# Optimization experiments

Measured on AMD Instinct MI355X. Metric: run time of the kernel, lower is better.

Reference implementation:

```python
import jax, jax.numpy as jnp
import numpy as np

N_NODES = 50000
N_EDGES = 1_600_000
IN_F = 128
OUT_F = 32
HEADS = 4
EDGE_F = 4
EDGE_HID = 32


def setup_inputs() -> dict:
    key = jax.random.key(0)
    ks = jax.random.split(key, 12)
    x = jax.random.normal(ks[0], (N_NODES, IN_F), dtype=jnp.float32)
    edge_index = jax.random.randint(ks[1], (2, N_EDGES), 0, N_NODES, dtype=jnp.int32)
    edge_attr = jax.random.normal(ks[2], (N_EDGES, EDGE_F), dtype=jnp.float32)
    # linear: in_features -> heads*out_features (stored as [in, out] for x @ W)
    W = jax.random.normal(ks[3], (IN_F, HEADS * OUT_F), dtype=jnp.float32) * (1.0 / np.sqrt(IN_F))
    b = jnp.zeros((HEADS * OUT_F,), dtype=jnp.float32)
    # edge_proj: Linear(EDGE_F,32) -> ReLU -> Linear(32, heads)
    eW1 = jax.random.normal(ks[4], (EDGE_F, EDGE_HID), dtype=jnp.float32) * (1.0 / np.sqrt(EDGE_F))
    eb1 = jnp.zeros((EDGE_HID,), dtype=jnp.float32)
    eW2 = jax.random.normal(ks[5], (EDGE_HID, HEADS), dtype=jnp.float32) * (1.0 / np.sqrt(EDGE_HID))
    eb2 = jnp.zeros((HEADS,), dtype=jnp.float32)
    att_src = jax.random.normal(ks[6], (1, HEADS, OUT_F), dtype=jnp.float32) * 0.1
    att_dst = jax.random.normal(ks[7], (1, HEADS, OUT_F), dtype=jnp.float32) * 0.1
    return {"x": x, "edge_index": edge_index, "edge_attr": edge_attr,
            "W": W, "b": b, "eW1": eW1, "eb1": eb1, "eW2": eW2, "eb2": eb2,
            "att_src": att_src, "att_dst": att_dst}


def reference(x, edge_index, edge_attr, W, b, eW1, eb1, eW2, eb2, att_src, att_dst):
    N = x.shape[0]
    src, dst = edge_index[0], edge_index[1]
    E = src.shape[0]

    h = (x @ W + b).reshape(N, HEADS, OUT_F)                     # [N,H,F]
    alpha_src = jnp.sum(h[src] * att_src, axis=-1)               # [E,H]
    alpha_dst = jnp.sum(h[dst] * att_dst, axis=-1)               # [E,H]
    edge_att = jax.nn.relu(edge_attr @ eW1 + eb1) @ eW2 + eb2    # [E,H]
    alpha = jax.nn.leaky_relu(alpha_src + alpha_dst + edge_att, negative_slope=0.2)

    # softmax_by_src: dense [N,H] buffer of -inf, scatter-set by src
    # softmax over the NODE axis, then gather back per edge.
    last = jax.ops.segment_max(jnp.arange(E, dtype=jnp.int32), src, num_segments=N)  # [N]
    valid = last >= 0
    dense = jnp.where(valid[:, None], alpha[jnp.clip(last, 0)], -jnp.inf)  # [N,H]
    dense = jax.nn.softmax(dense, axis=0)
    alpha_e = dense[src]                                         # [E,H]

    # dropout: module default training=False path (identity), eval mode
    # scatter-add aggregation: out[src] += h[dst] * alpha_e (all heads at once)
    msg = h[dst] * alpha_e[:, :, None]                           # [E,H,F]
    out = jnp.zeros_like(h).at[src].add(msg)                     # [N,H,F]
    return out.mean(axis=1)                                      # [N,F]
```

## Files before the change

### kernel.cpp

```cpp
#include <hip/hip_runtime.h>
#include <hip/hip_fp16.h>
#include <math.h>


#define SUPCAP 9216
#define AGG_CAP 2048
#define BIN_CHUNK 2048

__global__ __launch_bounds__(256, 3) void k_pre(
    const float* __restrict__ x, const float* __restrict__ W,
    const float* __restrict__ b, const float* __restrict__ att_src,
    const float* __restrict__ att_dst, __half* __restrict__ hbuf16,
    float* __restrict__ s_, float* __restrict__ t_,
    const int* __restrict__ src, const int* __restrict__ dst,
    int* __restrict__ bcur, unsigned* __restrict__ bin_y,
    unsigned* __restrict__ bin_e,
    int N, int E, int nsup, int ngemm, int nbin) {
  __shared__ __align__(16) float smem[12672];
  int tx = threadIdx.x;
  int bid = blockIdx.x;
  int mmin = (nbin < ngemm) ? nbin : ngemm;
  int m2 = 2 * mmin;
  bool isbin;
  int wid;
  if (bid < m2) { isbin = (bid & 1); wid = bid >> 1; }
  else { isbin = (nbin > ngemm); wid = mmin + (bid - m2); }

  if (isbin) {
    uint2* ebuf = (uint2*)smem;
    int* hist = (int*)(smem + 4096);
    int* bas  = hist + 256;
    int* curs = bas + 256;
    int* gpos = curs + 256;
    int e0 = wid * BIN_CHUNK;
    int n = E - e0; if (n > BIN_CHUNK) n = BIN_CHUNK;
    hist[tx] = 0;
    __syncthreads();
    for (int i = tx; i < n; i += 256) {
      atomicAdd(&hist[src[e0 + i] >> 8], 1);
    }
    __syncthreads();
    int v = hist[tx];
    bas[tx] = v;
    __syncthreads();
    for (int off = 1; off < 256; off <<= 1) {
      int t = (tx >= off) ? bas[tx - off] : 0;
      __syncthreads();
      bas[tx] += t;
      __syncthreads();
    }
    curs[tx] = bas[tx] - v;
    if (tx < nsup && v > 0) gpos[tx] = atomicAdd(&bcur[tx], v);
    __syncthreads();
    for (int i = tx; i < n; i += 256) {
      int e = e0 + i;
      int s = src[e], d = dst[e];
      int pos = atomicAdd(&curs[s >> 8], 1);
      unsigned loc = (unsigned)(s & 255);
      ebuf[pos] = make_uint2((loc << 24) | (unsigned)e, (loc << 16) | (unsigned)d);
    }
    __syncthreads();
    for (int i = tx; i < n; i += 256) {
      uint2 w = ebuf[i];
      int lo = 0, hi = 255;
      while (lo < hi) {
        int mid = (lo + hi) >> 1;
        if (bas[mid] > i) hi = mid; else lo = mid + 1;
      }
      int bb = lo;
      int lbase = bas[bb] - hist[bb];
      int off = gpos[bb] + (i - lbase);
      if (off < SUPCAP) {
        bin_e[(size_t)bb * SUPCAP + off] = w.x;
        bin_y[(size_t)bb * SUPCAP + off] = w.y;
      }
    }
  } else {
    float* xs = smem;
    float* ws = smem + 64 * 132;
    int r0 = wid * 64;
    const float4* xg = (const float4*)(x + (size_t)r0 * 128);
#pragma unroll
    for (int j = 0; j < 8; ++j) {
      int l = tx + j * 256;
      int row = l >> 5, col4 = l & 31;
      float4 v = make_float4(0.f, 0.f, 0.f, 0.f);
      if (r0 + row < N) v = xg[l];
      *(float4*)(xs + row * 132 + col4 * 4) = v;
    }
    int cg = tx & 15, rg = tx >> 4;
    float acc[4][8];
#pragma unroll
    for (int r = 0; r < 4; ++r)
#pragma unroll
      for (int c = 0; c < 8; ++c) acc[r][c] = 0.f;
    const float4* Wg4 = (const float4*)W;
    const float* xbase = xs + rg * 4 * 132;
    int woff = cg * 8 + ((cg >> 3) << 2);
    for (int kt = 0; kt < 4; ++kt) {
      __syncthreads();
#pragma unroll
      for (int j = 0; j < 4; ++j) {
        int ll = tx + j * 256;
        int row = ll >> 5, c4 = ll & 31;
        *(float4*)(ws + row * 132 + c4 * 4 + ((c4 >> 4) << 2)) = Wg4[kt * 1024 + ll];
      }
      __syncthreads();
#pragma unroll 2
      for (int k4 = 0; k4 < 8; ++k4) {
        float4 xr0 = *(const float4*)(xbase + kt * 32 + k4 * 4);
        float4 xr1 = *(const float4*)(xbase + 132 + kt * 32 + k4 * 4);
        float4 xr2 = *(const float4*)(xbase + 264 + kt * 32 + k4 * 4);
        float4 xr3 = *(const float4*)(xbase + 396 + kt * 32 + k4 * 4);
#pragma unroll
        for (int kk = 0; kk < 4; ++kk) {
          const float* wrow = ws + (k4 * 4 + kk) * 132 + woff;
          float4 w0 = *(const float4*)(wrow);
          float4 w1 = *(const float4*)(wrow + 4);
          const float wc[8] = {w0.x, w0.y, w0.z, w0.w, w1.x, w1.y, w1.z, w1.w};
          float xv0 = ((const float*)&xr0)[kk];
          float xv1 = ((const float*)&xr1)[kk];
          float xv2 = ((const float*)&xr2)[kk];
          float xv3 = ((const float*)&xr3)[kk];
#pragma unroll
          for (int c = 0; c < 8; ++c) {
            acc[0][c] += xv0 * wc[c];
            acc[1][c] += xv1 * wc[c];
            acc[2][c] += xv2 * wc[c];
            acc[3][c] += xv3 * wc[c];
          }
        }
      }
    }
    float4 b0 = ((const float4*)b)[cg * 2],       b1 = ((const float4*)b)[cg * 2 + 1];
    float4 s0 = ((const float4*)att_src)[cg * 2], s1 = ((const float4*)att_src)[cg * 2 + 1];
    float4 d0 = ((const float4*)att_dst)[cg * 2], d1 = ((const float4*)att_dst)[cg * 2 + 1];
    const float bbv[8] = {b0.x, b0.y, b0.z, b0.w, b1.x, b1.y, b1.z, b1.w};
    const float asv[8] = {s0.x, s0.y, s0.z, s0.w, s1.x, s1.y, s1.z, s1.w};
    const float adv[8] = {d0.x, d0.y, d0.z, d0.w, d1.x, d1.y, d1.z, d1.w};
    int hd = cg >> 2;
#pragma unroll
    for (int r = 0; r < 4; ++r) {
      float o[8];
#pragma unroll
      for (int c = 0; c < 8; ++c) o[c] = acc[r][c] + bbv[c];
      float sp = 0.f, tp = 0.f;
#pragma unroll
      for (int c = 0; c < 8; ++c) { sp += o[c] * asv[c]; tp += o[c] * adv[c]; }
      sp += __shfl_xor(sp, 1); sp += __shfl_xor(sp, 2);
      tp += __shfl_xor(tp, 1); tp += __shfl_xor(tp, 2);
      int grow = r0 + rg * 4 + r;
      if (grow < N) {
        __half2 h0 = __floats2half2_rn(o[0], o[1]);
        __half2 h1 = __floats2half2_rn(o[2], o[3]);
        __half2 h2 = __floats2half2_rn(o[4], o[5]);
        __half2 h3 = __floats2half2_rn(o[6], o[7]);
        uint4 u;
        u.x = *(unsigned*)&h0; u.y = *(unsigned*)&h1;
        u.z = *(unsigned*)&h2; u.w = *(unsigned*)&h3;
        ((uint4*)(hbuf16 + (size_t)grow * 128))[cg] = u;
        if ((tx & 3) == 0) {
          s_[grow * 4 + hd] = sp;
          t_[grow * 4 + hd] = tp;
        }
      }
    }
  }
}

__global__ __launch_bounds__(256) void k_dense(
    const int* __restrict__ bcur, const unsigned* __restrict__ bin_e,
    const unsigned* __restrict__ bin_y,
    const int* __restrict__ dst, const float* __restrict__ edge_attr,
    const float* __restrict__ eW1, const float* __restrict__ eb1,
    const float* __restrict__ eW2, const float* __restrict__ eb2,
    const float* __restrict__ s_, const float* __restrict__ t_,
    float* __restrict__ dense, float* __restrict__ pmax,
    float* __restrict__ psum,
    unsigned short* __restrict__ sorted_dst,
    int* __restrict__ noff, int* __restrict__ ncnt, int N) {
  __shared__ int lastv[256];
  __shared__ int hist[256], bas[256], curs[256];
  __shared__ float lm[256 * 4], ls[256 * 4];
  int sp = blockIdx.x, tx = threadIdx.x;
  lastv[tx] = -1;
  hist[tx] = 0;
  __syncthreads();
  int cnt = bcur[sp]; if (cnt > SUPCAP) cnt = SUPCAP;
  const unsigned* be = bin_e + (size_t)sp * SUPCAP;
  const unsigned* by = bin_y + (size_t)sp * SUPCAP;
  for (int i = tx; i < cnt; i += 256) {
    unsigned p = be[i];
    atomicMax(&lastv[p >> 24], (int)(p & 0xFFFFFF));
    atomicAdd(&hist[by[i] >> 16], 1);
  }
  __syncthreads();
  int v = hist[tx];
  bas[tx] = v;
  __syncthreads();
  for (int off = 1; off < 256; off <<= 1) {
    int t = (tx >= off) ? bas[tx - off] : 0;
    __syncthreads();
    bas[tx] += t;
    __syncthreads();
  }
  curs[tx] = bas[tx] - v;
  int gn = sp * 256 + tx;
  noff[gn] = sp * SUPCAP + bas[tx] - v;
  ncnt[gn] = v;
  __syncthreads();
  unsigned short* sd = sorted_dst + (size_t)sp * SUPCAP;
  for (int i = tx; i < cnt; i += 256) {
    unsigned y = by[i];
    int pos = atomicAdd(&curs[y >> 16], 1);
    sd[pos] = (unsigned short)y;
  }
  float vv[4] = {-INFINITY, -INFINITY, -INFINITY, -INFINITY};
  if (gn < N) {
    int e = lastv[tx];
    if (e >= 0) {
      int d = dst[e];
      const float* ea = edge_attr + (size_t)e * 4;
      float e0 = ea[0], e1 = ea[1], e2 = ea[2], e3 = ea[3];
      float a0 = eb2[0], a1 = eb2[1], a2 = eb2[2], a3 = eb2[3];
#pragma unroll
      for (int i = 0; i < 32; ++i) {
        float hid = eb1[i] + e0 * eW1[i] + e1 * eW1[32 + i] + e2 * eW1[64 + i] + e3 * eW1[96 + i];
        hid = fmaxf(hid, 0.f);
        a0 += hid * eW2[i * 4 + 0]; a1 += hid * eW2[i * 4 + 1];
        a2 += hid * eW2[i * 4 + 2]; a3 += hid * eW2[i * 4 + 3];
      }
      float w0 = s_[gn * 4 + 0] + t_[d * 4 + 0] + a0;
      float w1 = s_[gn * 4 + 1] + t_[d * 4 + 1] + a1;
      float w2 = s_[gn * 4 + 2] + t_[d * 4 + 2] + a2;
      float w3 = s_[gn * 4 + 3] + t_[d * 4 + 3] + a3;
      vv[0] = w0 > 0.f ? w0 : 0.2f * w0;
      vv[1] = w1 > 0.f ? w1 : 0.2f * w1;
      vv[2] = w2 > 0.f ? w2 : 0.2f * w2;
      vv[3] = w3 > 0.f ? w3 : 0.2f * w3;
    }
#pragma unroll
    for (int h = 0; h < 4; ++h) dense[gn * 4 + h] = vv[h];
  }
#pragma unroll
  for (int h = 0; h < 4; ++h) {
    lm[tx * 4 + h] = vv[h];
    ls[tx * 4 + h] = (vv[h] > -INFINITY) ? 1.f : 0.f;
  }
  __syncthreads();
  for (int off = 128; off > 0; off >>= 1) {
    if (tx < off) {
#pragma unroll
      for (int h = 0; h < 4; ++h) {
        float m2 = lm[(tx + off) * 4 + h], s2 = ls[(tx + off) * 4 + h];
        float m1 = lm[tx * 4 + h], s1 = ls[tx * 4 + h];
        float M = fmaxf(m1, m2);
        if (M > -INFINITY) {
          ls[tx * 4 + h] = s1 * expf(m1 - M) + s2 * expf(m2 - M);
          lm[tx * 4 + h] = M;
        }
      }
    }
    __syncthreads();
  }
  if (tx == 0) {
#pragma unroll
    for (int h = 0; h < 4; ++h) {
      pmax[sp * 4 + h] = lm[h];
      psum[sp * 4 + h] = ls[h];
    }
  }
}

#define ACC(r, P, Q) { \
  float2 f0 = __half22float2(*(__half2*)&r.x), f1 = __half22float2(*(__half2*)&r.y); \
  float2 f2 = __half22float2(*(__half2*)&r.z), f3 = __half22float2(*(__half2*)&r.w); \
  P.x += f0.x; P.y += f0.y; P.z += f1.x; P.w += f1.y; \
  Q.x += f2.x; Q.y += f2.y; Q.z += f3.x; Q.w += f3.y; }

__global__ __launch_bounds__(256) void k_agg(
    const unsigned short* __restrict__ sorted_dst,
    const int* __restrict__ noff, const int* __restrict__ ncnt,
    const __half* __restrict__ hbuf16, const float* __restrict__ dense,
    const float* __restrict__ pmax, const float* __restrict__ psum, int nb,
    float* __restrict__ out, int N) {
  __shared__ unsigned short sl[AGG_CAP];
  __shared__ float lm[256], ls[256];
  __shared__ float sgm[4], sgi[4];
  int tx = threadIdx.x;
  int n0 = blockIdx.x << 4;
  int nlast = n0 + 15; if (nlast > N - 1) nlast = N - 1;
  int lstart = noff[n0];
  int lend = noff[nlast] + ncnt[nlast];
  int total = lend - lstart; if (total > AGG_CAP) total = AGG_CAP;
  for (int i = tx; i < total; i += 256) sl[i] = sorted_dst[lstart + i];
  {
    int h = tx & 3, chunk = tx >> 2;
    float m = -INFINITY, s = 0.f;
    for (int bq = chunk; bq < nb; bq += 64) {
      float m2 = pmax[bq * 4 + h], s2 = psum[bq * 4 + h];
      float M = fmaxf(m, m2);
      if (M > -INFINITY) {
        s = s * expf(m - M) + s2 * expf(m2 - M);
        m = M;
      }
    }
    lm[tx] = m; ls[tx] = s;
    __syncthreads();
    for (int off = 128; off >= 4; off >>= 1) {
      if (tx < off) {
        float m2 = lm[tx + off], s2 = ls[tx + off];
        float m1 = lm[tx], s1 = ls[tx];
        float M = fmaxf(m1, m2);
        if (M > -INFINITY) {
          ls[tx] = s1 * expf(m1 - M) + s2 * expf(m2 - M);
          lm[tx] = M;
        }
      }
      __syncthreads();
    }
    if (tx < 4) {
      sgm[tx] = lm[tx];
      sgi[tx] = 1.f / ls[tx];
    }
    __syncthreads();
  }
  int g = tx >> 4, l = tx & 15;
  int n = n0 + g;
  if (n >= N) return;
  int beg = noff[n] - lstart;
  int cnt = ncnt[n];
  if (beg + cnt > total) cnt = total - beg;
  int end = beg + cnt;
  int hd = l >> 2;
  float w = expf(dense[(size_t)n * 4 + hd] - sgm[hd]) * sgi[hd];
  float4 p0 = {0, 0, 0, 0}, q0 = {0, 0, 0, 0};
  float4 p1 = {0, 0, 0, 0}, q1 = {0, 0, 0, 0};
  int e = beg;
  for (; e + 7 < end; e += 8) {
    int c0 = sl[e],     c1 = sl[e + 1], c2 = sl[e + 2], c3 = sl[e + 3];
    int c4_ = sl[e + 4], c5 = sl[e + 5], c6 = sl[e + 6], c7 = sl[e + 7];
    uint4 r0 = *((const uint4*)(hbuf16 + ((size_t)c0  << 7)) + l);
    uint4 r1 = *((const uint4*)(hbuf16 + ((size_t)c1  << 7)) + l);
    uint4 r2 = *((const uint4*)(hbuf16 + ((size_t)c2  << 7)) + l);
    uint4 r3 = *((const uint4*)(hbuf16 + ((size_t)c3  << 7)) + l);
    uint4 r4 = *((const uint4*)(hbuf16 + ((size_t)c4_ << 7)) + l);
    uint4 r5 = *((const uint4*)(hbuf16 + ((size_t)c5  << 7)) + l);
    uint4 r6 = *((const uint4*)(hbuf16 + ((size_t)c6  << 7)) + l);
    uint4 r7 = *((const uint4*)(hbuf16 + ((size_t)c7  << 7)) + l);
    ACC(r0, p0, q0); ACC(r1, p1, q1); ACC(r2, p0, q0); ACC(r3, p1, q1);
    ACC(r4, p0, q0); ACC(r5, p1, q1); ACC(r6, p0, q0); ACC(r7, p1, q1);
  }
  for (; e + 3 < end; e += 4) {
    int c0 = sl[e], c1 = sl[e + 1], c2 = sl[e + 2], c3 = sl[e + 3];
    uint4 r0 = *((const uint4*)(hbuf16 + ((size_t)c0 << 7)) + l);
    uint4 r1 = *((const uint4*)(hbuf16 + ((size_t)c1 << 7)) + l);
    uint4 r2 = *((const uint4*)(hbuf16 + ((size_t)c2 << 7)) + l);
    uint4 r3 = *((const uint4*)(hbuf16 + ((size_t)c3 << 7)) + l);
    ACC(r0, p0, q0); ACC(r1, p1, q1); ACC(r2, p0, q0); ACC(r3, p1, q1);
  }
  for (; e < end; ++e) {
    int c0 = sl[e];
    uint4 r0 = *((const uint4*)(hbuf16 + ((size_t)c0 << 7)) + l);
    ACC(r0, p0, q0);
  }
  p0.x += p1.x; p0.y += p1.y; p0.z += p1.z; p0.w += p1.w;
  q0.x += q1.x; q0.y += q1.y; q0.z += q1.z; q0.w += q1.w;
  p0.x *= w; p0.y *= w; p0.z *= w; p0.w *= w;
  q0.x *= w; q0.y *= w; q0.z *= w; q0.w *= w;
  p0.x += __shfl_xor(p0.x, 4);  p0.y += __shfl_xor(p0.y, 4);
  p0.z += __shfl_xor(p0.z, 4);  p0.w += __shfl_xor(p0.w, 4);
  q0.x += __shfl_xor(q0.x, 4);  q0.y += __shfl_xor(q0.y, 4);
  q0.z += __shfl_xor(q0.z, 4);  q0.w += __shfl_xor(q0.w, 4);
  p0.x += __shfl_xor(p0.x, 8);  p0.y += __shfl_xor(p0.y, 8);
  p0.z += __shfl_xor(p0.z, 8);  p0.w += __shfl_xor(p0.w, 8);
  q0.x += __shfl_xor(q0.x, 8);  q0.y += __shfl_xor(q0.y, 8);
  q0.z += __shfl_xor(q0.z, 8);  q0.w += __shfl_xor(q0.w, 8);
  if (l < 4) {
    float4 oA, oB;
    oA.x = 0.25f * p0.x; oA.y = 0.25f * p0.y; oA.z = 0.25f * p0.z; oA.w = 0.25f * p0.w;
    oB.x = 0.25f * q0.x; oB.y = 0.25f * q0.y; oB.z = 0.25f * q0.z; oB.w = 0.25f * q0.w;
    *(float4*)(out + (size_t)n * 32 + l * 8) = oA;
    *(float4*)(out + (size_t)n * 32 + l * 8 + 4) = oB;
  }
}

extern "C" void kernel_launch(void* const* d_in, const int* in_sizes, int n_in,
                              void* d_out, int out_size, void* d_ws, size_t ws_size,
                              hipStream_t stream) {
  const float* x        = (const float*)d_in[0];
  const int*   ei       = (const int*)d_in[1];
  const float* edge_attr= (const float*)d_in[2];
  const float* W        = (const float*)d_in[3];
  const float* b        = (const float*)d_in[4];
  const float* eW1      = (const float*)d_in[5];
  const float* eb1      = (const float*)d_in[6];
  const float* eW2      = (const float*)d_in[7];
  const float* eb2      = (const float*)d_in[8];
  const float* att_src  = (const float*)d_in[9];
  const float* att_dst  = (const float*)d_in[10];
  float* out = (float*)d_out;

  const int N = in_sizes[0] / 128;
  const int E = in_sizes[1] / 2;
  const int* src = ei;
  const int* dst = ei + E;
  const int NSUP = (N + 255) >> 8;

  char* wp = (char*)d_ws;
  auto alloc = [&](size_t bytes) -> void* {
    void* p = (void*)wp;
    wp += (bytes + 255) & ~(size_t)255;
    return p;
  };
  __half* hbuf16 = (__half*)alloc((size_t)N * 128 * 2);
  float* s_    = (float*)alloc((size_t)N * 4 * 4);
  float* t_    = (float*)alloc((size_t)N * 4 * 4);
  float* dense = (float*)alloc((size_t)N * 4 * 4);
  float* pmax  = (float*)alloc((size_t)NSUP * 4 * 4);
  float* psum  = (float*)alloc((size_t)NSUP * 4 * 4);
  int* bcur    = (int*)alloc((size_t)NSUP * 4);
  unsigned* bin_y = (unsigned*)alloc((size_t)NSUP * SUPCAP * 4);
  unsigned* bin_e = (unsigned*)alloc((size_t)NSUP * SUPCAP * 4);
  unsigned short* sorted_dst = (unsigned short*)alloc((size_t)NSUP * SUPCAP * 2);
  int* noff    = (int*)alloc((size_t)NSUP * 256 * 4);
  int* ncnt    = (int*)alloc((size_t)NSUP * 256 * 4);

  const int NGEMM = (N + 63) / 64;
  const int NBIN  = (E + BIN_CHUNK - 1) / BIN_CHUNK;

  hipMemsetAsync(bcur, 0, (size_t)NSUP * 4, stream);
  k_pre<<<NGEMM + NBIN, 256, 0, stream>>>(x, W, b, att_src, att_dst, hbuf16, s_, t_,
                                          src, dst, bcur, bin_y, bin_e,
                                          N, E, NSUP, NGEMM, NBIN);
  k_dense<<<NSUP, 256, 0, stream>>>(bcur, bin_e, bin_y, dst, edge_attr, eW1, eb1, eW2, eb2,
                                    s_, t_, dense, pmax, psum, sorted_dst, noff, ncnt, N);
  k_agg<<<(N + 15) / 16, 256, 0, stream>>>(sorted_dst, noff, ncnt, hbuf16, dense,
                                           pmax, psum, NSUP, out, N);
}
```

Baseline: 239.3 us.

## Fuse three kernels into one persistent kernel with software grid barriers

Merges the GEMM/binning, dense softmax, and aggregation kernels into a single persistent kernel sized to occupancy times CU count. Work items are grid-strided and phases are separated by an atomic-counter grid barrier, removing two kernel launch gaps and their tail effects. The GEMM tile shrinks from 64 to 32 rows to fit reduced shared memory and allow 4 blocks per CU. The risk is barrier spin overhead and load imbalance, plus deadlock if not all blocks are co-resident.

```diff
diff --git a/kernel.cpp b/kernel.cpp
--- a/kernel.cpp
+++ b/kernel.cpp
@@ -7,381 +7,404 @@
 #define AGG_CAP 2048
 #define BIN_CHUNK 2048
 
-__global__ __launch_bounds__(256, 3) void k_pre(
+__device__ __forceinline__ void gsync(int* bar, int nblk) {
+  __syncthreads();
+  if (threadIdx.x == 0) {
+    __threadfence();
+    int g = __hip_atomic_load(&bar[1], __ATOMIC_RELAXED, __HIP_MEMORY_SCOPE_AGENT);
+    int a = __hip_atomic_fetch_add(&bar[0], 1, __ATOMIC_ACQ_REL, __HIP_MEMORY_SCOPE_AGENT);
+    if (a == nblk - 1) {
+      __hip_atomic_store(&bar[0], 0, __ATOMIC_RELAXED, __HIP_MEMORY_SCOPE_AGENT);
+      __hip_atomic_fetch_add(&bar[1], 1, __ATOMIC_RELEASE, __HIP_MEMORY_SCOPE_AGENT);
+    } else {
+      while (__hip_atomic_load(&bar[1], __ATOMIC_ACQUIRE, __HIP_MEMORY_SCOPE_AGENT) == g)
+        __builtin_amdgcn_s_sleep(8);
+    }
+    __threadfence();
+  }
+  __syncthreads();
+}
+
+#define ACC(r, P, Q) { \
+  float2 f0 = __half22float2(*(__half2*)&r.x), f1 = __half22float2(*(__half2*)&r.y); \
+  float2 f2 = __half22float2(*(__half2*)&r.z), f3 = __half22float2(*(__half2*)&r.w); \
+  P.x += f0.x; P.y += f0.y; P.z += f1.x; P.w += f1.y; \
+  Q.x += f2.x; Q.y += f2.y; Q.z += f3.x; Q.w += f3.y; }
+
+__global__ __launch_bounds__(256, 4) void k_fused(
     const float* __restrict__ x, const float* __restrict__ W,
     const float* __restrict__ b, const float* __restrict__ att_src,
     const float* __restrict__ att_dst, __half* __restrict__ hbuf16,
     float* __restrict__ s_, float* __restrict__ t_,
     const int* __restrict__ src, const int* __restrict__ dst,
+    const float* __restrict__ edge_attr,
+    const float* __restrict__ eW1, const float* __restrict__ eb1,
+    const float* __restrict__ eW2, const float* __restrict__ eb2,
     int* __restrict__ bcur, unsigned* __restrict__ bin_y,
     unsigned* __restrict__ bin_e,
-    int N, int E, int nsup, int ngemm, int nbin) {
-  __shared__ __align__(16) float smem[12672];
-  int tx = threadIdx.x;
-  int bid = blockIdx.x;
-  int mmin = (nbin < ngemm) ? nbin : ngemm;
-  int m2 = 2 * mmin;
-  bool isbin;
-  int wid;
-  if (bid < m2) { isbin = (bid & 1); wid = bid >> 1; }
-  else { isbin = (nbin > ngemm); wid = mmin + (bid - m2); }
-
-  if (isbin) {
-    uint2* ebuf = (uint2*)smem;
-    int* hist = (int*)(smem + 4096);
-    int* bas  = hist + 256;
-    int* curs = bas + 256;
-    int* gpos = curs + 256;
-    int e0 = wid * BIN_CHUNK;
-    int n = E - e0; if (n > BIN_CHUNK) n = BIN_CHUNK;
-    hist[tx] = 0;
-    __syncthreads();
-    for (int i = tx; i < n; i += 256) {
-      atomicAdd(&hist[src[e0 + i] >> 8], 1);
-    }
-    __syncthreads();
-    int v = hist[tx];
-    bas[tx] = v;
-    __syncthreads();
-    for (int off = 1; off < 256; off <<= 1) {
-      int t = (tx >= off) ? bas[tx - off] : 0;
-      __syncthreads();
-      bas[tx] += t;
-      __syncthreads();
-    }
-    curs[tx] = bas[tx] - v;
-    if (tx < nsup && v > 0) gpos[tx] = atomicAdd(&bcur[tx], v);
-    __syncthreads();
-    for (int i = tx; i < n; i += 256) {
-      int e = e0 + i;
-      int s = src[e], d = dst[e];
-      int pos = atomicAdd(&curs[s >> 8], 1);
-      unsigned loc = (unsigned)(s & 255);
-      ebuf[pos] = make_uint2((loc << 24) | (unsigned)e, (loc << 16) | (unsigned)d);
-    }
-    __syncthreads();
-    for (int i = tx; i < n; i += 256) {
-      uint2 w = ebuf[i];
-      int lo = 0, hi = 255;
-      while (lo < hi) {
-        int mid = (lo + hi) >> 1;
-        if (bas[mid] > i) hi = mid; else lo = mid + 1;
-      }
-      int bb = lo;
-      int lbase = bas[bb] - hist[bb];
-      int off = gpos[bb] + (i - lbase);
-      if (off < SUPCAP) {
-        bin_e[(size_t)bb * SUPCAP + off] = w.x;
-        bin_y[(size_t)bb * SUPCAP + off] = w.y;
-      }
-    }
-  } else {
-    float* xs = smem;
-    float* ws = smem + 64 * 132;
-    int r0 = wid * 64;
-    const float4* xg = (const float4*)(x + (size_t)r0 * 128);
-#pragma unroll
-    for (int j = 0; j < 8; ++j) {
-      int l = tx + j * 256;
-      int row = l >> 5, col4 = l & 31;
-      float4 v = make_float4(0.f, 0.f, 0.f, 0.f);
-      if (r0 + row < N) v = xg[l];
-      *(float4*)(xs + row * 132 + col4 * 4) = v;
-    }
-    int cg = tx & 15, rg = tx >> 4;
-    float acc[4][8];
-#pragma unroll
-    for (int r = 0; r < 4; ++r)
-#pragma unroll
-      for (int c = 0; c < 8; ++c) acc[r][c] = 0.f;
-    const float4* Wg4 = (const float4*)W;
-    const float* xbase = xs + rg * 4 * 132;
-    int woff = cg * 8 + ((cg >> 3) << 2);
-    for (int kt = 0; kt < 4; ++kt) {
-      __syncthreads();
-#pragma unroll
-      for (int j = 0; j < 4; ++j) {
-        int ll = tx + j * 256;
-        int row = ll >> 5, c4 = ll & 31;
-        *(float4*)(ws + row * 132 + c4 * 4 + ((c4 >> 4) << 2)) = Wg4[kt * 1024 + ll];
-      }
-      __syncthreads();
-#pragma unroll 2
-      for (int k4 = 0; k4 < 8; ++k4) {
-        float4 xr0 = *(const float4*)(xbase + kt * 32 + k4 * 4);
-        float4 xr1 = *(const float4*)(xbase + 132 + kt * 32 + k4 * 4);
-        float4 xr2 = *(const float4*)(xbase + 264 + kt * 32 + k4 * 4);
-        float4 xr3 = *(const float4*)(xbase + 396 + kt * 32 + k4 * 4);
-#pragma unroll
-        for (int kk = 0; kk < 4; ++kk) {
-          const float* wrow = ws + (k4 * 4 + kk) * 132 + woff;
-          float4 w0 = *(const float4*)(wrow);
-          float4 w1 = *(const float4*)(wrow + 4);
-          const float wc[8] = {w0.x, w0.y, w0.z, w0.w, w1.x, w1.y, w1.z, w1.w};
-          float xv0 = ((const float*)&xr0)[kk];
-          float xv1 = ((const float*)&xr1)[kk];
-          float xv2 = ((const float*)&xr2)[kk];
-          float xv3 = ((const float*)&xr3)[kk];
-#pragma unroll
-          for (int c = 0; c < 8; ++c) {
-            acc[0][c] += xv0 * wc[c];
-            acc[1][c] += xv1 * wc[c];
-            acc[2][c] += xv2 * wc[c];
-            acc[3][c] += xv3 * wc[c];
-          }
-        }
-      }
-    }
-    float4 b0 = ((const float4*)b)[cg * 2],       b1 = ((const float4*)b)[cg * 2 + 1];
-    float4 s0 = ((const float4*)att_src)[cg * 2], s1 = ((const float4*)att_src)[cg * 2 + 1];
-    float4 d0 = ((const float4*)att_dst)[cg * 2], d1 = ((const float4*)att_dst)[cg * 2 + 1];
-    const float bbv[8] = {b0.x, b0.y, b0.z, b0.w, b1.x, b1.y, b1.z, b1.w};
-    const float asv[8] = {s0.x, s0.y, s0.z, s0.w, s1.x, s1.y, s1.z, s1.w};
-    const float adv[8] = {d0.x, d0.y, d0.z, d0.w, d1.x, d1.y, d1.z, d1.w};
-    int hd = cg >> 2;
-#pragma unroll
-    for (int r = 0; r < 4; ++r) {
-      float o[8];
-#pragma unroll
-      for (int c = 0; c < 8; ++c) o[c] = acc[r][c] + bbv[c];
-      float sp = 0.f, tp = 0.f;
-#pragma unroll
-      for (int c = 0; c < 8; ++c) { sp += o[c] * asv[c]; tp += o[c] * adv[c]; }
-      sp += __shfl_xor(sp, 1); sp += __shfl_xor(sp, 2);
-      tp += __shfl_xor(tp, 1); tp += __shfl_xor(tp, 2);
-      int grow = r0 + rg * 4 + r;
-      if (grow < N) {
-        __half2 h0 = __floats2half2_rn(o[0], o[1]);
-        __half2 h1 = __floats2half2_rn(o[2], o[3]);
-        __half2 h2 = __floats2half2_rn(o[4], o[5]);
-        __half2 h3 = __floats2half2_rn(o[6], o[7]);
-        uint4 u;
-        u.x = *(unsigned*)&h0; u.y = *(unsigned*)&h1;
-        u.z = *(unsigned*)&h2; u.w = *(unsigned*)&h3;
-        ((uint4*)(hbuf16 + (size_t)grow * 128))[cg] = u;
-        if ((tx & 3) == 0) {
-          s_[grow * 4 + hd] = sp;
-          t_[grow * 4 + hd] = tp;
-        }
-      }
-    }
-  }
-}
-
-__global__ __launch_bounds__(256) void k_dense(
-    const int* __restrict__ bcur, const unsigned* __restrict__ bin_e,
-    const unsigned* __restrict__ bin_y,
-    const int* __restrict__ dst, const float* __restrict__ edge_attr,
-    const float* __restrict__ eW1, const float* __restrict__ eb1,
-    const float* __restrict__ eW2, const float* __restrict__ eb2,
-    const float* __restrict__ s_, const float* __restrict__ t_,
+    unsigned short* __restrict__ sorted_dst,
+    int* __restrict__ noff, int* __restrict__ ncnt,
     float* __restrict__ dense, float* __restrict__ pmax,
-    float* __restrict__ psum,
-    unsigned short* __restrict__ sorted_dst,
-    int* __restrict__ noff, int* __restrict__ ncnt, int N) {
-  __shared__ int lastv[256];
-  __shared__ int hist[256], bas[256], curs[256];
-  __shared__ float lm[256 * 4], ls[256 * 4];
-  int sp = blockIdx.x, tx = threadIdx.x;
-  lastv[tx] = -1;
-  hist[tx] = 0;
-  __syncthreads();
-  int cnt = bcur[sp]; if (cnt > SUPCAP) cnt = SUPCAP;
-  const unsigned* be = bin_e + (size_t)sp * SUPCAP;
-  const unsigned* by = bin_y + (size_t)sp * SUPCAP;
-  for (int i = tx; i < cnt; i += 256) {
-    unsigned p = be[i];
-    atomicMax(&lastv[p >> 24], (int)(p & 0xFFFFFF));
-    atomicAdd(&hist[by[i] >> 16], 1);
-  }
-  __syncthreads();
-  int v = hist[tx];
-  bas[tx] = v;
-  __syncthreads();
-  for (int off = 1; off < 256; off <<= 1) {
-    int t = (tx >= off) ? bas[tx - off] : 0;
-    __syncthreads();
-    bas[tx] += t;
-    __syncthreads();
-  }
-  curs[tx] = bas[tx] - v;
-  int gn = sp * 256 + tx;
-  noff[gn] = sp * SUPCAP + bas[tx] - v;
-  ncnt[gn] = v;
-  __syncthreads();
-  unsigned short* sd = sorted_dst + (size_t)sp * SUPCAP;
-  for (int i = tx; i < cnt; i += 256) {
-    unsigned y = by[i];
-    int pos = atomicAdd(&curs[y >> 16], 1);
-    sd[pos] = (unsigned short)y;
-  }
-  float vv[4] = {-INFINITY, -INFINITY, -INFINITY, -INFINITY};
-  if (gn < N) {
-    int e = lastv[tx];
-    if (e >= 0) {
-      int d = dst[e];
-      const float* ea = edge_attr + (size_t)e * 4;
-      float e0 = ea[0], e1 = ea[1], e2 = ea[2], e3 = ea[3];
-      float a0 = eb2[0], a1 = eb2[1], a2 = eb2[2], a3 = eb2[3];
-#pragma unroll
-      for (int i = 0; i < 32; ++i) {
-        float hid = eb1[i] + e0 * eW1[i] + e1 * eW1[32 + i] + e2 * eW1[64 + i] + e3 * eW1[96 + i];
-        hid = fmaxf(hid, 0.f);
-        a0 += hid * eW2[i * 4 + 0]; a1 += hid * eW2[i * 4 + 1];
-        a2 += hid * eW2[i * 4 + 2]; a3 += hid * eW2[i * 4 + 3];
-      }
-      float w0 = s_[gn * 4 + 0] + t_[d * 4 + 0] + a0;
-      float w1 = s_[gn * 4 + 1] + t_[d * 4 + 1] + a1;
-      float w2 = s_[gn * 4 + 2] + t_[d * 4 + 2] + a2;
-      float w3 = s_[gn * 4 + 3] + t_[d * 4 + 3] + a3;
-      vv[0] = w0 > 0.f ? w0 : 0.2f * w0;
-      vv[1] = w1 > 0.f ? w1 : 0.2f * w1;
-      vv[2] = w2 > 0.f ? w2 : 0.2f * w2;
-      vv[3] = w3 > 0.f ? w3 : 0.2f * w3;
-    }
-#pragma unroll
-    for (int h = 0; h < 4; ++h) dense[gn * 4 + h] = vv[h];
-  }
-#pragma unroll
-  for (int h = 0; h < 4; ++h) {
-    lm[tx * 4 + h] = vv[h];
-    ls[tx * 4 + h] = (vv[h] > -INFINITY) ? 1.f : 0.f;
-  }
-  __syncthreads();
-  for (int off = 128; off > 0; off >>= 1) {
-    if (tx < off) {
-#pragma unroll
-      for (int h = 0; h < 4; ++h) {
-        float m2 = lm[(tx + off) * 4 + h], s2 = ls[(tx + off) * 4 + h];
-        float m1 = lm[tx * 4 + h], s1 = ls[tx * 4 + h];
-        float M = fmaxf(m1, m2);
-        if (M > -INFINITY) {
-          ls[tx * 4 + h] = s1 * expf(m1 - M) + s2 * expf(m2 - M);
-          lm[tx * 4 + h] = M;
-        }
-      }
-    }
-    __syncthreads();
-  }
-  if (tx == 0) {
-#pragma unroll
-    for (int h = 0; h < 4; ++h) {
-      pmax[sp * 4 + h] = lm[h];
-      psum[sp * 4 + h] = ls[h];
-    }
-  }
-}
-
-#define ACC(r, P, Q) { \
-  float2 f0 = __half22float2(*(__half2*)&r.x), f1 = __half22float2(*(__half2*)&r.y); \
-  float2 f2 = __half22float2(*(__half2*)&r.z), f3 = __half22float2(*(__half2*)&r.w); \
-  P.x += f0.x; P.y += f0.y; P.z += f1.x; P.w += f1.y; \
-  Q.x += f2.x; Q.y += f2.y; Q.z += f3.x; Q.w += f3.y; }
-
-__global__ __launch_bounds__(256) void k_agg(
-    const unsigned short* __restrict__ sorted_dst,
-    const int* __restrict__ noff, const int* __restrict__ ncnt,
-    const __half* __restrict__ hbuf16, const float* __restrict__ dense,
-    const float* __restrict__ pmax, const float* __restrict__ psum, int nb,
-    float* __restrict__ out, int N) {
-  __shared__ unsigned short sl[AGG_CAP];
-  __shared__ float lm[256], ls[256];
+    float* __restrict__ psum, float* __restrict__ out,
+    int N, int E, int nsup, int ngemm, int nbin, int nagg,
+    int phases, int* bar) {
+  __shared__ __align__(16) float smem[8448];
   __shared__ float sgm[4], sgi[4];
   int tx = threadIdx.x;
-  int n0 = blockIdx.x << 4;
-  int nlast = n0 + 15; if (nlast > N - 1) nlast = N - 1;
-  int lstart = noff[n0];
-  int lend = noff[nlast] + ncnt[nlast];
-  int total = lend - lstart; if (total > AGG_CAP) total = AGG_CAP;
-  for (int i = tx; i < total; i += 256) sl[i] = sorted_dst[lstart + i];
-  {
-    int h = tx & 3, chunk = tx >> 2;
-    float m = -INFINITY, s = 0.f;
-    for (int bq = chunk; bq < nb; bq += 64) {
-      float m2 = pmax[bq * 4 + h], s2 = psum[bq * 4 + h];
-      float M = fmaxf(m, m2);
-      if (M > -INFINITY) {
-        s = s * expf(m - M) + s2 * expf(m2 - M);
-        m = M;
+  int bid = blockIdx.x, G = gridDim.x;
+  bool fused = (phases == 7);
+
+  if (phases & 1) {
+    int nitems = ngemm + nbin;
+    int mmin = (nbin < ngemm) ? nbin : ngemm;
+    int m2 = 2 * mmin;
+    for (int j = bid; j < nitems; j += G) {
+      __syncthreads();
+      bool isbin; int wid;
+      if (j < m2) { isbin = (j & 1); wid = j >> 1; }
+      else { isbin = (nbin > ngemm); wid = mmin + (j - m2); }
+      if (isbin) {
+        uint2* ebuf = (uint2*)smem;
+        int* hist = (int*)(smem + 4096);
+        int* bas  = hist + 256;
+        int* curs = bas + 256;
+        int* gpos = curs + 256;
+        int e0 = wid * BIN_CHUNK;
+        int n = E - e0; if (n > BIN_CHUNK) n = BIN_CHUNK;
+        hist[tx] = 0;
+        __syncthreads();
+        for (int i = tx; i < n; i += 256) {
+          atomicAdd(&hist[src[e0 + i] >> 8], 1);
+        }
+        __syncthreads();
+        int v = hist[tx];
+        bas[tx] = v;
+        __syncthreads();
+        for (int off = 1; off < 256; off <<= 1) {
+          int t = (tx >= off) ? bas[tx - off] : 0;
+          __syncthreads();
+          bas[tx] += t;
+          __syncthreads();
+        }
+        curs[tx] = bas[tx] - v;
+        if (tx < nsup && v > 0) gpos[tx] = atomicAdd(&bcur[tx], v);
+        __syncthreads();
+        for (int i = tx; i < n; i += 256) {
+          int e = e0 + i;
+          int s = src[e], d = dst[e];
+          int pos = atomicAdd(&curs[s >> 8], 1);
+          unsigned loc = (unsigned)(s & 255);
+          ebuf[pos] = make_uint2((loc << 24) | (unsigned)e, (loc << 16) | (unsigned)d);
+        }
+        __syncthreads();
+        for (int i = tx; i < n; i += 256) {
+          uint2 w = ebuf[i];
+          int lo = 0, hi = 255;
+          while (lo < hi) {
+            int mid = (lo + hi) >> 1;
+            if (bas[mid] > i) hi = mid; else lo = mid + 1;
+          }
+          int bb = lo;
+          int lbase = bas[bb] - hist[bb];
+          int off = gpos[bb] + (i - lbase);
+          if (off < SUPCAP) {
+            bin_e[(size_t)bb * SUPCAP + off] = w.x;
+            bin_y[(size_t)bb * SUPCAP + off] = w.y;
+          }
+        }
+      } else {
+        float* xs = smem;
+        float* ws = smem + 4224;
+        int r0 = wid * 32;
+        const float4* xg = (const float4*)(x + (size_t)r0 * 128);
+#pragma unroll
+        for (int j2 = 0; j2 < 4; ++j2) {
+          int l = tx + j2 * 256;
+          int row = l >> 5, col4 = l & 31;
+          float4 v = make_float4(0.f, 0.f, 0.f, 0.f);
+          if (r0 + row < N) v = xg[l];
+          *(float4*)(xs + row * 132 + col4 * 4) = v;
+        }
+        int cg = tx & 15, rg = tx >> 4;
+        float acc[2][8];
+#pragma unroll
+        for (int r = 0; r < 2; ++r)
+#pragma unroll
+          for (int c = 0; c < 8; ++c) acc[r][c] = 0.f;
+        const float4* Wg4 = (const float4*)W;
+        const float* xbase = xs + rg * 2 * 132;
+        int woff = cg * 8 + ((cg >> 3) << 2);
+        for (int kt = 0; kt < 4; ++kt) {
+          __syncthreads();
+#pragma unroll
+          for (int j2 = 0; j2 < 4; ++j2) {
+            int ll = tx + j2 * 256;
+            int row = ll >> 5, c4 = ll & 31;
+            *(float4*)(ws + row * 132 + c4 * 4 + ((c4 >> 4) << 2)) = Wg4[kt * 1024 + ll];
+          }
+          __syncthreads();
+#pragma unroll 2
+          for (int k4 = 0; k4 < 8; ++k4) {
+            float4 xr0 = *(const float4*)(xbase + kt * 32 + k4 * 4);
+            float4 xr1 = *(const float4*)(xbase + 132 + kt * 32 + k4 * 4);
+#pragma unroll
+            for (int kk = 0; kk < 4; ++kk) {
+              const float* wrow = ws + (k4 * 4 + kk) * 132 + woff;
+              float4 w0 = *(const float4*)(wrow);
+              float4 w1 = *(const float4*)(wrow + 4);
+              const float wc[8] = {w0.x, w0.y, w0.z, w0.w, w1.x, w1.y, w1.z, w1.w};
+              float xv0 = ((const float*)&xr0)[kk];
+              float xv1 = ((const float*)&xr1)[kk];
+#pragma unroll
+              for (int c = 0; c < 8; ++c) {
+                acc[0][c] += xv0 * wc[c];
+                acc[1][c] += xv1 * wc[c];
+              }
+            }
+          }
+        }
+        float4 b0 = ((const float4*)b)[cg * 2],       b1 = ((const float4*)b)[cg * 2 + 1];
+        float4 s0 = ((const float4*)att_src)[cg * 2], s1 = ((const float4*)att_src)[cg * 2 + 1];
+        float4 d0 = ((const float4*)att_dst)[cg * 2], d1 = ((const float4*)att_dst)[cg * 2 + 1];
+        const float bbv[8] = {b0.x, b0.y, b0.z, b0.w, b1.x, b1.y, b1.z, b1.w};
+        const float asv[8] = {s0.x, s0.y, s0.z, s0.w, s1.x, s1.y, s1.z, s1.w};
+        const float adv[8] = {d0.x, d0.y, d0.z, d0.w, d1.x, d1.y, d1.z, d1.w};
+        int hd = cg >> 2;
+#pragma unroll
+        for (int r = 0; r < 2; ++r) {
+          float o[8];
+#pragma unroll
+          for (int c = 0; c < 8; ++c) o[c] = acc[r][c] + bbv[c];
+          float sp = 0.f, tp = 0.f;
+#pragma unroll
+          for (int c = 0; c < 8; ++c) { sp += o[c] * asv[c]; tp += o[c] * adv[c]; }
+          sp += __shfl_xor(sp, 1); sp += __shfl_xor(sp, 2);
+          tp += __shfl_xor(tp, 1); tp += __shfl_xor(tp, 2);
+          int grow = r0 + rg * 2 + r;
+          if (grow < N) {
+            __half2 h0 = __floats2half2_rn(o[0], o[1]);
+            __half2 h1 = __floats2half2_rn(o[2], o[3]);
+            __half2 h2 = __floats2half2_rn(o[4], o[5]);
+            __half2 h3 = __floats2half2_rn(o[6], o[7]);
+            uint4 u;
+            u.x = *(unsigned*)&h0; u.y = *(unsigned*)&h1;
+            u.z = *(unsigned*)&h2; u.w = *(unsigned*)&h3;
+            ((uint4*)(hbuf16 + (size_t)grow * 128))[cg] = u;
+            if ((tx & 3) == 0) {
+              s_[grow * 4 + hd] = sp;
+              t_[grow * 4 + hd] = tp;
+            }
+          }
+        }
       }
     }
-    lm[tx] = m; ls[tx] = s;
-    __syncthreads();
-    for (int off = 128; off >= 4; off >>= 1) {
-      if (tx < off) {
-        float m2 = lm[tx + off], s2 = ls[tx + off];
-        float m1 = lm[tx], s1 = ls[tx];
-        float M = fmaxf(m1, m2);
+  }
+  if (fused) gsync(bar, G);
+
+  if (phases & 2) {
+    int* lastv = (int*)smem;
+    int* hist  = (int*)(smem + 256);
+    int* bas   = (int*)(smem + 512);
+    int* curs  = (int*)(smem + 768);
+    float* lm  = smem + 1024;
+    float* ls  = smem + 2048;
+    for (int sp = bid; sp < nsup; sp += G) {
+      __syncthreads();
+      lastv[tx] = -1;
+      hist[tx] = 0;
+      __syncthreads();
+      int cnt = bcur[sp]; if (cnt > SUPCAP) cnt = SUPCAP;
+      const unsigned* be = bin_e + (size_t)sp * SUPCAP;
+      const unsigned* by = bin_y + (size_t)sp * SUPCAP;
+      for (int i = tx; i < cnt; i += 256) {
+        unsigned p = be[i];
+        atomicMax(&lastv[p >> 24], (int)(p & 0xFFFFFF));
+        atomicAdd(&hist[by[i] >> 16], 1);
+      }
+      __syncthreads();
+      int v = hist[tx];
+      bas[tx] = v;
+      __syncthreads();
+      for (int off = 1; off < 256; off <<= 1) {
+        int t = (tx >= off) ? bas[tx - off] : 0;
+        __syncthreads();
+        bas[tx] += t;
+        __syncthreads();
+      }
+      curs[tx] = bas[tx] - v;
+      int gn = sp * 256 + tx;
+      noff[gn] = sp * SUPCAP + bas[tx] - v;
+      ncnt[gn] = v;
+      __syncthreads();
+      unsigned short* sd = sorted_dst + (size_t)sp * SUPCAP;
+      for (int i = tx; i < cnt; i += 256) {
+        unsigned y = by[i];
+        int pos = atomicAdd(&curs[y >> 16], 1);
+        sd[pos] = (unsigned short)y;
+      }
+      float vv[4] = {-INFINITY, -INFINITY, -INFINITY, -INFINITY};
+      if (gn < N) {
+        int e = lastv[tx];
+        if (e >= 0) {
+          int d = dst[e];
+          const float* ea = edge_attr + (size_t)e * 4;
+          float e0 = ea[0], e1 = ea[1], e2 = ea[2], e3 = ea[3];
+          float a0 = eb2[0], a1 = eb2[1], a2 = eb2[2], a3 = eb2[3];
+#pragma unroll
+          for (int i = 0; i < 32; ++i) {
+            float hid = eb1[i] + e0 * eW1[i] + e1 * eW1[32 + i] + e2 * eW1[64 + i] + e3 * eW1[96 + i];
+            hid = fmaxf(hid, 0.f);
+            a0 += hid * eW2[i * 4 + 0]; a1 += hid * eW2[i * 4 + 1];
+            a2 += hid * eW2[i * 4 + 2]; a3 += hid * eW2[i * 4 + 3];
+          }
+          float w0 = s_[gn * 4 + 0] + t_[d * 4 + 0] + a0;
+          float w1 = s_[gn * 4 + 1] + t_[d * 4 + 1] + a1;
+          float w2 = s_[gn * 4 + 2] + t_[d * 4 + 2] + a2;
+          float w3 = s_[gn * 4 + 3] + t_[d * 4 + 3] + a3;
+          vv[0] = w0 > 0.f ? w0 : 0.2f * w0;
+          vv[1] = w1 > 0.f ? w1 : 0.2f * w1;
+          vv[2] = w2 > 0.f ? w2 : 0.2f * w2;
+          vv[3] = w3 > 0.f ? w3 : 0.2f * w3;
+        }
+#pragma unroll
+        for (int h = 0; h < 4; ++h) dense[gn * 4 + h] = vv[h];
+      }
+#pragma unroll
+      for (int h = 0; h < 4; ++h) {
+        lm[tx * 4 + h] = vv[h];
+        ls[tx * 4 + h] = (vv[h] > -INFINITY) ? 1.f : 0.f;
+      }
+      __syncthreads();
+      for (int off = 128; off > 0; off >>= 1) {
+        if (tx < off) {
+#pragma unroll
+          for (int h = 0; h < 4; ++h) {
+            float m2 = lm[(tx + off) * 4 + h], s2 = ls[(tx + off) * 4 + h];
+            float m1 = lm[tx * 4 + h], s1 = ls[tx * 4 + h];
+            float M = fmaxf(m1, m2);
+            if (M > -INFINITY) {
+              ls[tx * 4 + h] = s1 * expf(m1 - M) + s2 * expf(m2 - M);
+              lm[tx * 4 + h] = M;
+            }
+          }
+        }
+        __syncthreads();
+      }
+      if (tx == 0) {
+#pragma unroll
+        for (int h = 0; h < 4; ++h) {
+          pmax[sp * 4 + h] = lm[h];
+          psum[sp * 4 + h] = ls[h];
+        }
+      }
+    }
+  }
+  if (fused) gsync(bar, G);
+
+  if (phases & 4) {
+    {
+      float* lm = smem + 1024;
+      float* ls = smem + 1280;
+      int h = tx & 3, chunk = tx >> 2;
+      float m = -INFINITY, s = 0.f;
+      for (int bq = chunk; bq < nsup; bq += 64) {
+        float m2 = pmax[bq * 4 + h], s2 = psum[bq * 4 + h];
+        float M = fmaxf(m, m2);
         if (M > -INFINITY) {
-          ls[tx] = s1 * expf(m1 - M) + s2 * expf(m2 - M);
-          lm[tx] = M;
-        }
+          s = s * expf(m - M) + s2 * expf(m2 - M);
+          m = M;
+        }
+      }
+      lm[tx] = m; ls[tx] = s;
+      __syncthreads();
+      for (int off = 128; off >= 4; off >>= 1) {
+        if (tx < off) {
+          float m2 = lm[tx + off], s2 = ls[tx + off];
+          float m1 = lm[tx], s1 = ls[tx];
+          float M = fmaxf(m1, m2);
+          if (M > -INFINITY) {
+            ls[tx] = s1 * expf(m1 - M) + s2 * expf(m2 - M);
+            lm[tx] = M;
+          }
+        }
+        __syncthreads();
+      }
+      if (tx < 4) {
+        sgm[tx] = lm[tx];
+        sgi[tx] = 1.f / ls[tx];
       }
       __syncthreads();
     }
-    if (tx < 4) {
-      sgm[tx] = lm[tx];
-      sgi[tx] = 1.f / ls[tx];
+    unsigned short* sl = (unsigned short*)smem;
+    for (int it = bid; it < nagg; it += G) {
+      __syncthreads();
+      int n0 = it << 4;
+      int nlast = n0 + 15; if (nlast > N - 1) nlast = N - 1;
+      int lstart = noff[n0];
+      int lend = noff[nlast] + ncnt[nlast];
+      int total = lend - lstart; if (total > AGG_CAP) total = AGG_CAP;
+      for (int i = tx; i < total; i += 256) sl[i] = sorted_dst[lstart + i];
+      __syncthreads();
+      int g = tx >> 4, l = tx & 15;
+      int n = n0 + g;
+      if (n < N) {
+        int beg = noff[n] - lstart;
+        int cnt = ncnt[n];
+        if (beg + cnt > total) cnt = total - beg;
+        int end = beg + cnt;
+        int hd = l >> 2;
+        float w = expf(dense[(size_t)n * 4 + hd] - sgm[hd]) * sgi[hd];
+        float4 p0 = {0, 0, 0, 0}, q0 = {0, 0, 0, 0};
+        float4 p1 = {0, 0, 0, 0}, q1 = {0, 0, 0, 0};
+        int e = beg;
+        for (; e + 7 < end; e += 8) {
+          int c0 = sl[e],     c1 = sl[e + 1], c2 = sl[e + 2], c3 = sl[e + 3];
+          int c4_ = sl[e + 4], c5 = sl[e + 5], c6 = sl[e + 6], c7 = sl[e + 7];
+          uint4 r0 = *((const uint4*)(hbuf16 + ((size_t)c0  << 7)) + l);
+          uint4 r1 = *((const uint4*)(hbuf16 + ((size_t)c1  << 7)) + l);
+          uint4 r2 = *((const uint4*)(hbuf16 + ((size_t)c2  << 7)) + l);
+          uint4 r3 = *((const uint4*)(hbuf16 + ((size_t)c3  << 7)) + l);
+          uint4 r4 = *((const uint4*)(hbuf16 + ((size_t)c4_ << 7)) + l);
+          uint4 r5 = *((const uint4*)(hbuf16 + ((size_t)c5  << 7)) + l);
+          uint4 r6 = *((const uint4*)(hbuf16 + ((size_t)c6  << 7)) + l);
+          uint4 r7 = *((const uint4*)(hbuf16 + ((size_t)c7  << 7)) + l);
+          ACC(r0, p0, q0); ACC(r1, p1, q1); ACC(r2, p0, q0); ACC(r3, p1, q1);
+          ACC(r4, p0, q0); ACC(r5, p1, q1); ACC(r6, p0, q0); ACC(r7, p1, q1);
+        }
+        for (; e + 3 < end; e += 4) {
+          int c0 = sl[e], c1 = sl[e + 1], c2 = sl[e + 2], c3 = sl[e + 3];
+          uint4 r0 = *((const uint4*)(hbuf16 + ((size_t)c0 << 7)) + l);
+          uint4 r1 = *((const uint4*)(hbuf16 + ((size_t)c1 << 7)) + l);
+          uint4 r2 = *((const uint4*)(hbuf16 + ((size_t)c2 << 7)) + l);
+          uint4 r3 = *((const uint4*)(hbuf16 + ((size_t)c3 << 7)) + l);
+          ACC(r0, p0, q0); ACC(r1, p1, q1); ACC(r2, p0, q0); ACC(r3, p1, q1);
+        }
+        for (; e < end; ++e) {
+          int c0 = sl[e];
+          uint4 r0 = *((const uint4*)(hbuf16 + ((size_t)c0 << 7)) + l);
+          ACC(r0, p0, q0);
+        }
+        p0.x += p1.x; p0.y += p1.y; p0.z += p1.z; p0.w += p1.w;
+        q0.x += q1.x; q0.y += q1.y; q0.z += q1.z; q0.w += q1.w;
+        p0.x *= w; p0.y *= w; p0.z *= w; p0.w *= w;
+        q0.x *= w; q0.y *= w; q0.z *= w; q0.w *= w;
+        p0.x += __shfl_xor(p0.x, 4);  p0.y += __shfl_xor(p0.y, 4);
+        p0.z += __shfl_xor(p0.z, 4);  p0.w += __shfl_xor(p0.w, 4);
+        q0.x += __shfl_xor(q0.x, 4);  q0.y += __shfl_xor(q0.y, 4);
+        q0.z += __shfl_xor(q0.z, 4);  q0.w += __shfl_xor(q0.w, 4);
+        p0.x += __shfl_xor(p0.x, 8);  p0.y += __shfl_xor(p0.y, 8);
+        p0.z += __shfl_xor(p0.z, 8);  p0.w += __shfl_xor(p0.w, 8);
+        q0.x += __shfl_xor(q0.x, 8);  q0.y += __shfl_xor(q0.y, 8);
+        q0.z += __shfl_xor(q0.z, 8);  q0.w += __shfl_xor(q0.w, 8);
+        if (l < 4) {
+          float4 oA, oB;
+          oA.x = 0.25f * p0.x; oA.y = 0.25f * p0.y; oA.z = 0.25f * p0.z; oA.w = 0.25f * p0.w;
+          oB.x = 0.25f * q0.x; oB.y = 0.25f * q0.y; oB.z = 0.25f * q0.z; oB.w = 0.25f * q0.w;
+          *(float4*)(out + (size_t)n * 32 + l * 8) = oA;
+          *(float4*)(out + (size_t)n * 32 + l * 8 + 4) = oB;
+        }
+      }
     }
-    __syncthreads();
-  }
-  int g = tx >> 4, l = tx & 15;
-  int n = n0 + g;
-  if (n >= N) return;
-  int beg = noff[n] - lstart;
-  int cnt = ncnt[n];
-  if (beg + cnt > total) cnt = total - beg;
-  int end = beg + cnt;
-  int hd = l >> 2;
-  float w = expf(dense[(size_t)n * 4 + hd] - sgm[hd]) * sgi[hd];
-  float4 p0 = {0, 0, 0, 0}, q0 = {0, 0, 0, 0};
-  float4 p1 = {0, 0, 0, 0}, q1 = {0, 0, 0, 0};
-  int e = beg;
-  for (; e + 7 < end; e += 8) {
-    int c0 = sl[e],     c1 = sl[e + 1], c2 = sl[e + 2], c3 = sl[e + 3];
-    int c4_ = sl[e + 4], c5 = sl[e + 5], c6 = sl[e + 6], c7 = sl[e + 7];
-    uint4 r0 = *((const uint4*)(hbuf16 + ((size_t)c0  << 7)) + l);
-    uint4 r1 = *((const uint4*)(hbuf16 + ((size_t)c1  << 7)) + l);
-    uint4 r2 = *((const uint4*)(hbuf16 + ((size_t)c2  << 7)) + l);
-    uint4 r3 = *((const uint4*)(hbuf16 + ((size_t)c3  << 7)) + l);
-    uint4 r4 = *((const uint4*)(hbuf16 + ((size_t)c4_ << 7)) + l);
-    uint4 r5 = *((const uint4*)(hbuf16 + ((size_t)c5  << 7)) + l);
-    uint4 r6 = *((const uint4*)(hbuf16 + ((size_t)c6  << 7)) + l);
-    uint4 r7 = *((const uint4*)(hbuf16 + ((size_t)c7  << 7)) + l);
-    ACC(r0, p0, q0); ACC(r1, p1, q1); ACC(r2, p0, q0); ACC(r3, p1, q1);
-    ACC(r4, p0, q0); ACC(r5, p1, q1); ACC(r6, p0, q0); ACC(r7, p1, q1);
-  }
-  for (; e + 3 < end; e += 4) {
-    int c0 = sl[e], c1 = sl[e + 1], c2 = sl[e + 2], c3 = sl[e + 3];
-    uint4 r0 = *((const uint4*)(hbuf16 + ((size_t)c0 << 7)) + l);
-    uint4 r1 = *((const uint4*)(hbuf16 + ((size_t)c1 << 7)) + l);
-    uint4 r2 = *((const uint4*)(hbuf16 + ((size_t)c2 << 7)) + l);
-    uint4 r3 = *((const uint4*)(hbuf16 + ((size_t)c3 << 7)) + l);
-    ACC(r0, p0, q0); ACC(r1, p1, q1); ACC(r2, p0, q0); ACC(r3, p1, q1);
-  }
-  for (; e < end; ++e) {
-    int c0 = sl[e];
-    uint4 r0 = *((const uint4*)(hbuf16 + ((size_t)c0 << 7)) + l);
-    ACC(r0, p0, q0);
-  }
-  p0.x += p1.x; p0.y += p1.y; p0.z += p1.z; p0.w += p1.w;
-  q0.x += q1.x; q0.y += q1.y; q0.z += q1.z; q0.w += q1.w;
-  p0.x *= w; p0.y *= w; p0.z *= w; p0.w *= w;
-  q0.x *= w; q0.y *= w; q0.z *= w; q0.w *= w;
-  p0.x += __shfl_xor(p0.x, 4);  p0.y += __shfl_xor(p0.y, 4);
-  p0.z += __shfl_xor(p0.z, 4);  p0.w += __shfl_xor(p0.w, 4);
-  q0.x += __shfl_xor(q0.x, 4);  q0.y += __shfl_xor(q0.y, 4);
-  q0.z += __shfl_xor(q0.z, 4);  q0.w += __shfl_xor(q0.w, 4);
-  p0.x += __shfl_xor(p0.x, 8);  p0.y += __shfl_xor(p0.y, 8);
-  p0.z += __shfl_xor(p0.z, 8);  p0.w += __shfl_xor(p0.w, 8);
-  q0.x += __shfl_xor(q0.x, 8);  q0.y += __shfl_xor(q0.y, 8);
-  q0.z += __shfl_xor(q0.z, 8);  q0.w += __shfl_xor(q0.w, 8);
-  if (l < 4) {
-    float4 oA, oB;
-    oA.x = 0.25f * p0.x; oA.y = 0.25f * p0.y; oA.z = 0.25f * p0.z; oA.w = 0.25f * p0.w;
-    oB.x = 0.25f * q0.x; oB.y = 0.25f * q0.y; oB.z = 0.25f * q0.z; oB.w = 0.25f * q0.w;
-    *(float4*)(out + (size_t)n * 32 + l * 8) = oA;
-    *(float4*)(out + (size_t)n * 32 + l * 8 + 4) = oB;
   }
 }
 
@@ -419,22 +442,50 @@
   float* dense = (float*)alloc((size_t)N * 4 * 4);
   float* pmax  = (float*)alloc((size_t)NSUP * 4 * 4);
   float* psum  = (float*)alloc((size_t)NSUP * 4 * 4);
-  int* bcur    = (int*)alloc((size_t)NSUP * 4);
+  int* bcur    = (int*)alloc((size_t)(NSUP + 2) * 4);
   unsigned* bin_y = (unsigned*)alloc((size_t)NSUP * SUPCAP * 4);
   unsigned* bin_e = (unsigned*)alloc((size_t)NSUP * SUPCAP * 4);
   unsigned short* sorted_dst = (unsigned short*)alloc((size_t)NSUP * SUPCAP * 2);
   int* noff    = (int*)alloc((size_t)NSUP * 256 * 4);
   int* ncnt    = (int*)alloc((size_t)NSUP * 256 * 4);
-
-  const int NGEMM = (N + 63) / 64;
+  int* bar     = bcur + NSUP;
+
+  const int NGEMM = (N + 31) / 32;
   const int NBIN  = (E + BIN_CHUNK - 1) / BIN_CHUNK;
-
-  hipMemsetAsync(bcur, 0, (size_t)NSUP * 4, stream);
-  k_pre<<<NGEMM + NBIN, 256, 0, stream>>>(x, W, b, att_src, att_dst, hbuf16, s_, t_,
-                                          src, dst, bcur, bin_y, bin_e,
-                                          N, E, NSUP, NGEMM, NBIN);
-  k_dense<<<NSUP, 256, 0, stream>>>(bcur, bin_e, bin_y, dst, edge_attr, eW1, eb1, eW2, eb2,
-                                    s_, t_, dense, pmax, psum, sorted_dst, noff, ncnt, N);
-  k_agg<<<(N + 15) / 16, 256, 0, stream>>>(sorted_dst, noff, ncnt, hbuf16, dense,
-                                           pmax, psum, NSUP, out, N);
+  const int NAGG  = (N + 15) / 16;
+
+  static int g_grid = -1;
+  if (g_grid < 0) {
+    int dev = 0, occ = 0, ncu = 0;
+    hipError_t e1 = hipGetDevice(&dev);
+    hipDeviceProp_t prop;
+    hipError_t e2 = hipGetDeviceProperties(&prop, dev);
+    hipError_t e3 = hipOccupancyMaxActiveBlocksPerMultiprocessor(&occ, k_fused, 256, 0);
+    ncu = prop.multiProcessorCount;
+    if (e1 == hipSuccess && e2 == hipSuccess && e3 == hipSuccess && occ >= 1 && ncu >= 1)
+      g_grid = occ * ncu;
+    else
+      g_grid = 0;
+  }
+
+  hipMemsetAsync(bcur, 0, (size_t)(NSUP + 2) * 4, stream);
+  if (g_grid > 0) {
+    k_fused<<<g_grid, 256, 0, stream>>>(
+        x, W, b, att_src, att_dst, hbuf16, s_, t_, src, dst, edge_attr,
+        eW1, eb1, eW2, eb2, bcur, bin_y, bin_e, sorted_dst, noff, ncnt,
+        dense, pmax, psum, out, N, E, NSUP, NGEMM, NBIN, NAGG, 7, bar);
+  } else {
+    k_fused<<<NGEMM + NBIN, 256, 0, stream>>>(
+        x, W, b, att_src, att_dst, hbuf16, s_, t_, src, dst, edge_attr,
+        eW1, eb1, eW2, eb2, bcur, bin_y, bin_e, sorted_dst, noff, ncnt,
+        dense, pmax, psum, out, N, E, NSUP, NGEMM, NBIN, NAGG, 1, bar);
+    k_fused<<<NSUP, 256, 0, stream>>>(
+        x, W, b, att_src, att_dst, hbuf16, s_, t_, src, dst, edge_attr,
+        eW1, eb1, eW2, eb2, bcur, bin_y, bin_e, sorted_dst, noff, ncnt,
+        dense, pmax, psum, out, N, E, NSUP, NGEMM, NBIN, NAGG, 2, bar);
+    k_fused<<<NAGG, 256, 0, stream>>>(
+        x, W, b, att_src, att_dst, hbuf16, s_, t_, src, dst, edge_attr,
+        eW1, eb1, eW2, eb2, bcur, bin_y, bin_e, sorted_dst, noff, ncnt,
+        dense, pmax, psum, out, N, E, NSUP, NGEMM, NBIN, NAGG, 4, bar);
+  }
 }
```

Result: slower. 622.0 us (+159.9%).
